# Optimization experiments

Measured on AMD Instinct MI355X. Metric: run time of the kernel, lower is better.

## Reference

```python
import math
import jax, jax.numpy as jnp
import numpy as np

B, NH, L0 = 16, 128, 16384
KS, STRIDE = 4, 2
INIT_GATE_BIAS = 1.0


def _num_steps(L, ks, stride):
    # number of reduce steps until any N <= L reaches N <= 1 (matches torch N recurrence)
    d, n = 0, L
    while True:
        n = (max(n - ks, 0) + stride - 1) // stride + 1
        d += 1
        if n <= 1:
            return d


def setup_inputs() -> dict:
    key = jax.random.key(0)
    k1, k2, k3, k4 = jax.random.split(key, 4)
    h = jax.random.normal(k1, (B, NH, L0), dtype=jnp.float32)
    N = jax.random.randint(k2, (B,), 1, L0 + 1, dtype=jnp.int32)
    cin = NH + 1  # depth_variant adds one channel
    bound = 1.0 / math.sqrt(cin * KS)
    W = jax.random.uniform(k3, (3 * NH, cin, KS), minval=-bound, maxval=bound, dtype=jnp.float32)
    b = jax.random.uniform(k4, (3 * NH,), minval=-bound, maxval=bound, dtype=jnp.float32)
    b = b.at[2 * NH:].set(INIT_GATE_BIAS)
    return {"h": h, "N": N, "W": W, "b": b}


def _step(h, N, depth, W, b):
    Bb, _, Lc = h.shape
    # depth channel (depth_variant=True), then mask invalid positions (mask applied after concat, as in torch)
    d = jnp.full((Bb, 1, Lc), math.log1p(depth), dtype=h.dtype)
    hh = jnp.concatenate([h, d], axis=1)
    mask = (jnp.arange(Lc) < N[:, None]).astype(hh.dtype)  # [B, Lc]
    hh = hh * mask[:, None, :]
    # right-pad so conv covers all valid positions
    if Lc < KS:
        pad_r = KS - Lc
    elif (Lc - KS) % STRIDE != 0:
        pad_r = STRIDE - (Lc - KS) % STRIDE
    else:
        pad_r = 0
    if pad_r:
        hh = jnp.pad(hh, ((0, 0), (0, 0), (0, pad_r)))
    lrg = jax.lax.conv_general_dilated(
        hh, W, window_strides=(STRIDE,), padding='VALID',
        dimension_numbers=('NCH', 'OIH', 'NCH')) + b[None, :, None]
    l = lrg[:, :NH]
    r = jnp.tanh(lrg[:, NH:2 * NH])
    g = jax.nn.sigmoid(lrg[:, 2 * NH:])
    h_new = l * g + r * (1.0 - g)
    m = jnp.maximum(N - KS, 0)
    N_new = (m + STRIDE - 1) // STRIDE + 1  # ceil(clamp(N-ks,0)/stride)+1
    return h_new, N_new


def reference(h, N, W, b):
    # Fixed-depth unroll: instead of compacting the batch (dynamic shapes), run
    # every sample for all D steps and record its row at the step it finishes.
    # Torch output order = samples sorted stably by finish depth (boolean-index
    # compaction preserves original relative order), reproduced via stable argsort.
    D = _num_steps(h.shape[2], KS, STRIDE)
    Bb = h.shape[0]
    out_h = jnp.zeros((Bb, NH), dtype=h.dtype)
    finish = jnp.full((Bb,), D, dtype=jnp.int32)
    done = jnp.zeros((Bb,), dtype=bool)
    for depth in range(D):
        h, N = _step(h, N, depth, W, b)
        newly = (~done) & (N <= 1)
        out_h = jnp.where(newly[:, None], h[:, :, 0], out_h)
        finish = jnp.where(newly, depth, finish)
        done = done | newly
    order = jnp.argsort(finish)  # stable by default in jax
    return out_h[order]
```

## Files before the change

kernel.cpp:

```cpp
#include <hip/hip_runtime.h>
#include <math.h>

typedef _Float16 f16_t;
typedef _Float16 f16x8 __attribute__((ext_vector_type(8)));
typedef _Float16 f16x4 __attribute__((ext_vector_type(4)));
typedef float    f32x4 __attribute__((ext_vector_type(4)));

#define NHC 128
#define NBATCH 16
#define JT 64
#define THREADS 512
#define L0LEN 16384
#define LDSROWPITCH 272
#define LDSREGION (66*LDSROWPITCH)
#define TREGION (130*LDSROWPITCH)

__device__ __host__ __forceinline__ int nstep_f(int n){ int m = n - 4; m = m < 0 ? 0 : m; return ((m + 1) >> 1) + 1; }

__global__ void prep_kernel(const float* __restrict__ W, const float* __restrict__ bin,
                            f16_t* __restrict__ Wt, float* __restrict__ Pp, float* __restrict__ biasf)
{
    int c = blockIdx.x;
    int i = threadIdx.x;
    #pragma unroll
    for (int k = 0; k < 4; k++)
        Wt[((size_t)k*384 + c)*128 + i] = (f16_t)W[((size_t)c*129 + i)*4 + k];
    if (i == 0) {
        float s = 0.f;
        Pp[c*5 + 0] = 0.f;
        #pragma unroll
        for (int k = 0; k < 4; k++) { s += W[((size_t)c*129 + 128)*4 + k]; Pp[c*5 + k + 1] = s; }
        biasf[c] = bin[c];
    }
}

template<int REG, int CTM>
__device__ __forceinline__ void gemm_tap(f32x4 (&acc)[3][4], const f16_t* __restrict__ Wt,
                                         const char* ldsIn, int arow, int n16, int q, int jt)
{
    #pragma unroll 1
    for (int k = 0; k < 4; k++) {
        const f16_t* ab = Wt + ((size_t)k*384 + arow)*128 + q*8;
        f16x8 a0[4], a1[4], a2[4];
        #pragma unroll
        for (int kc = 0; kc < 4; kc++) {
            a0[kc] = *(const f16x8*)(ab + kc*32);
            a1[kc] = *(const f16x8*)(ab + 16384 + kc*32);
            a2[kc] = *(const f16x8*)(ab + 32768 + kc*32);
        }
        const char* bb0 = ldsIn + (k&1)*REG + ((k>>1) + n16 + jt*16)*LDSROWPITCH + q*16;
        #pragma unroll
        for (int kc = 0; kc < 4; kc++) {
            #pragma unroll
            for (int ct = 0; ct < CTM; ct++) {
                f16x8 bb = *(const f16x8*)(bb0 + ct*(16*LDSROWPITCH) + kc*64);
                acc[0][ct] = __builtin_amdgcn_mfma_f32_16x16x32_f16(a0[kc], bb, acc[0][ct], 0, 0, 0);
                acc[1][ct] = __builtin_amdgcn_mfma_f32_16x16x32_f16(a1[kc], bb, acc[1][ct], 0, 0, 0);
                acc[2][ct] = __builtin_amdgcn_mfma_f32_16x16x32_f16(a2[kc], bb, acc[2][ct], 0, 0, 0);
            }
        }
    }
}

__device__ __forceinline__ void load_biasp(float (&biasr)[3][4], float (&pfull)[3][4],
                                           const float* __restrict__ biasf,
                                           const float* __restrict__ Pp, int cw)
{
    #pragma unroll
    for (int s = 0; s < 3; s++)
        #pragma unroll
        for (int r = 0; r < 4; r++) {
            int row = s*128 + cw + r;
            biasr[s][r] = biasf[row];
            pfull[s][r] = Pp[row*5 + 4];
        }
}

template<int REG, int CTE, bool TO_LDS>
__device__ __forceinline__ void epilogue_store(
    const f32x4 (&acc)[3][4], char* ldsOut, f16_t* goutB,
    const float (&biasr)[3][4], const float (&pfull)[3][4],
    const float* __restrict__ Pp, float* __restrict__ outrow,
    int j0, int Nt, int Nt1, float dval, bool record, int n16, int cw)
{
    #pragma unroll
    for (int ct = 0; ct < CTE; ct++) {
        int j = j0 + ct*16 + n16;
        int cnt = Nt - 2*j; cnt = cnt < 0 ? 0 : (cnt > 4 ? 4 : cnt);
        bool zero = (j >= Nt1);
        float hv[4];
        #pragma unroll
        for (int r = 0; r < 4; r++) {
            float d0, d1, d2;
            if (cnt == 4)      { d0 = pfull[0][r]; d1 = pfull[1][r]; d2 = pfull[2][r]; }
            else if (cnt == 0) { d0 = 0.f; d1 = 0.f; d2 = 0.f; }
            else { int rw = cw + r; d0 = Pp[rw*5 + cnt]; d1 = Pp[(128+rw)*5 + cnt]; d2 = Pp[(256+rw)*5 + cnt]; }
            float lv = acc[0][ct][r] + biasr[0][r] + dval*d0;
            float rp = acc[1][ct][r] + biasr[1][r] + dval*d1;
            float gp = acc[2][ct][r] + biasr[2][r] + dval*d2;
            float e2 = __expf(2.f*rp);
            float rv = 1.f - 2.f/(e2 + 1.f);
            float gv = 1.f/(1.f + __expf(-gp));
            float hh = lv*gv + rv*(1.f - gv);
            hv[r] = zero ? 0.f : hh;
        }
        f16x4 hb;
        #pragma unroll
        for (int r = 0; r < 4; r++) hb[r] = (f16_t)hv[r];
        if constexpr (TO_LDS) {
            *(f16x4*)(ldsOut + (j&1)*REG + (j>>1)*LDSROWPITCH + cw*2) = hb;
        } else {
            *(f16x4*)(goutB + (ct*16 + n16)*NHC + cw) = hb;
        }
        if (record && ct == 0 && n16 == 0) {
            #pragma unroll
            for (int r = 0; r < 4; r++) outrow[cw + r] = hv[r];
        }
    }
}

__global__ __launch_bounds__(THREADS) void conv_kernel(
    const float* __restrict__ h, const f16_t* __restrict__ Xin, f16_t* __restrict__ Xout,
    const f16_t* __restrict__ Wt, const float* __restrict__ Pp,
    const float* __restrict__ biasf, const int* __restrict__ N0,
    float* __restrict__ outbuf,
    int t, int inCols, int outCols, float dval)
{
    __shared__ alignas(16) char ldsX[2*LDSREGION];
    const int b  = blockIdx.y;
    const int j0 = blockIdx.x * JT;
    const int tid = threadIdx.x;
    int Nt = N0[b];
    for (int s = 0; s < t; s++) Nt = nstep_f(Nt);
    const int Nt1 = nstep_f(Nt);

    f16_t* XoutB = Xout + ((size_t)b*outCols + j0)*NHC;
    if (j0 >= Nt1) {
        float4 z = {0.f,0.f,0.f,0.f};
        float4* p = (float4*)XoutB;
        #pragma unroll
        for (int i = 0; i < 2; i++) p[i*THREADS + tid] = z;
        return;
    }

    if (t == 0) {
        const float* hB = h + (size_t)b*NHC*L0LEN;
        const int P0 = 2*j0;
        const int jpr = tid & 63;
        const int s8  = tid >> 6;
        #pragma unroll
        for (int cg = 0; cg < 16; cg++) {
            int c = cg*8 + s8;
            int p = P0 + jpr*2;
            float2 v = {0.f, 0.f};
            if (p + 1 < Nt)      v = *(const float2*)(hB + (size_t)c*L0LEN + p);
            else if (p < Nt)     v.x = hB[(size_t)c*L0LEN + p];
            char* wb = ldsX + jpr*LDSROWPITCH + c*2;
            *(f16_t*)(wb)             = (f16_t)v.x;
            *(f16_t*)(wb + LDSREGION) = (f16_t)v.y;
        }
        if (tid < 128) {
            int c = tid;
            int p = P0 + 128;
            float2 v = {0.f, 0.f};
            if (p + 1 < Nt)      v = *(const float2*)(hB + (size_t)c*L0LEN + p);
            else if (p < Nt)     v.x = hB[(size_t)c*L0LEN + p];
            char* wb = ldsX + 64*LDSROWPITCH + c*2;
            *(f16_t*)(wb)             = (f16_t)v.x;
            *(f16_t*)(wb + LDSREGION) = (f16_t)v.y;
        }
    } else {
        const char* XinB = (const char*)(Xin + ((size_t)b*inCols + 2*(size_t)j0)*NHC);
        const int maxrow = inCols - 2*j0;
        for (int it = 0; it < 5; ++it) {
            int idx = it*THREADS + tid;
            if (idx < 130*16) {
                int row = idx >> 4, cb = (idx & 15) * 16;
                float4 v = {0.f,0.f,0.f,0.f};
                if (row < maxrow) v = *(const float4*)(XinB + row*256 + cb);
                *(float4*)(ldsX + (row&1)*LDSREGION + (row>>1)*LDSROWPITCH + cb) = v;
            }
        }
    }
    __syncthreads();

    const int w    = tid >> 6;
    const int lane = tid & 63;
    const int n16  = lane & 15;
    const int q    = lane >> 4;
    const int arow = w*16 + n16;
    const int cw   = w*16 + q*4;

    f32x4 acc[3][4] = {};
    int ctm = (Nt1 - j0 + 15) >> 4; if (ctm > 4) ctm = 4;
    switch (ctm) {
    case 1:  gemm_tap<LDSREGION,1>(acc, Wt, ldsX, arow, n16, q, 0); break;
    case 2:  gemm_tap<LDSREGION,2>(acc, Wt, ldsX, arow, n16, q, 0); break;
    case 3:  gemm_tap<LDSREGION,3>(acc, Wt, ldsX, arow, n16, q, 0); break;
    default: gemm_tap<LDSREGION,4>(acc, Wt, ldsX, arow, n16, q, 0); break;
    }

    float biasr[3][4], pfull[3][4];
    load_biasp(biasr, pfull, biasf, Pp, cw);

    bool newly = (Nt1 == 1) && (t == 0 || Nt > 1);
    epilogue_store<LDSREGION,4,false>(acc, nullptr, XoutB, biasr, pfull, Pp, outbuf + b*NHC,
                                      j0, Nt, Nt1, dval, newly && (j0 == 0), n16, cw);
}

template<int REG, int CTM>
__device__ __forceinline__ void tail_iter(
    char* ldsX, const f16_t* __restrict__ Wt,
    const float (&biasr)[3][4], const float (&pfull)[3][4],
    const float* __restrict__ Pp, float* __restrict__ outrow,
    int n16, int q, int arow, int cw, int jt, int Nt, int Nt1, float dval, bool newly)
{
    f32x4 acc[3][4] = {};
    gemm_tap<REG,CTM>(acc, Wt, ldsX, arow, n16, q, jt);
    __syncthreads();
    epilogue_store<REG,CTM,true>(acc, ldsX, nullptr, biasr, pfull, Pp, outrow,
                                 jt*16, Nt, Nt1, dval, newly, n16, cw);
}

__global__ __launch_bounds__(THREADS) void tail_kernel(
    const f16_t* __restrict__ Xin, const f16_t* __restrict__ Wt,
    const float* __restrict__ Pp, const float* __restrict__ biasf,
    const int* __restrict__ N0, float* __restrict__ outbuf, int inCols)
{
    __shared__ alignas(16) char ldsX[2*TREGION];
    const int b = blockIdx.x;
    const int tid = threadIdx.x;
    int Nt = N0[b];
    for (int s = 0; s < 6; s++) Nt = nstep_f(Nt);
    if (Nt <= 1) return;

    const int w    = tid >> 6;
    const int lane = tid & 63;
    const int n16  = lane & 15;
    const int q    = lane >> 4;
    const int arow = w*16 + n16;
    const int cw   = w*16 + q*4;
    float* outrow  = outbuf + b*NHC;

    const char* XinB = (const char*)(Xin + (size_t)b*inCols*NHC);
    for (int it = 0; it < 8; ++it) {
        int idx = it*THREADS + tid;
        int row = idx >> 4, cb = (idx & 15) * 16;
        float4 v = {0.f,0.f,0.f,0.f};
        if (row < inCols) v = *(const float4*)(XinB + row*256 + cb);
        *(float4*)(ldsX + (row&1)*TREGION + (row>>1)*LDSROWPITCH + cb) = v;
    }

    float biasr[3][4], pfull[3][4];
    load_biasp(biasr, pfull, biasf, Pp, cw);
    __syncthreads();

    for (int t = 6; t < 13; ++t) {
        int Nt1 = nstep_f(Nt);
        bool newly = (Nt1 == 1);
        float dval = log1pf((float)t);
        int ctmax = (Nt1 >> 4) + 1; if (ctmax > 8) ctmax = 8;
        int cA = ctmax > 4 ? 4 : ctmax;
        switch (cA) {
        case 1:  tail_iter<TREGION,1>(ldsX, Wt, biasr, pfull, Pp, outrow, n16, q, arow, cw, 0, Nt, Nt1, dval, newly); break;
        case 2:  tail_iter<TREGION,2>(ldsX, Wt, biasr, pfull, Pp, outrow, n16, q, arow, cw, 0, Nt, Nt1, dval, newly); break;
        case 3:  tail_iter<TREGION,3>(ldsX, Wt, biasr, pfull, Pp, outrow, n16, q, arow, cw, 0, Nt, Nt1, dval, newly); break;
        default: tail_iter<TREGION,4>(ldsX, Wt, biasr, pfull, Pp, outrow, n16, q, arow, cw, 0, Nt, Nt1, dval, newly); break;
        }
        if (ctmax > 4) {
            switch (ctmax - 4) {
            case 1:  tail_iter<TREGION,1>(ldsX, Wt, biasr, pfull, Pp, outrow, n16, q, arow, cw, 4, Nt, Nt1, dval, false); break;
            case 2:  tail_iter<TREGION,2>(ldsX, Wt, biasr, pfull, Pp, outrow, n16, q, arow, cw, 4, Nt, Nt1, dval, false); break;
            case 3:  tail_iter<TREGION,3>(ldsX, Wt, biasr, pfull, Pp, outrow, n16, q, arow, cw, 4, Nt, Nt1, dval, false); break;
            default: tail_iter<TREGION,4>(ldsX, Wt, biasr, pfull, Pp, outrow, n16, q, arow, cw, 4, Nt, Nt1, dval, false); break;
            }
        }
        if (newly) return;
        Nt = Nt1;
        __syncthreads();
    }
}

__global__ void finalize_kernel(const float* __restrict__ outbuf,
                                const int* __restrict__ N0, float* __restrict__ dout)
{
    __shared__ int fin[16];
    __shared__ int rnk[16];
    int tid = threadIdx.x;
    if (tid < 16) {
        int n = N0[tid]; int f = 12;
        for (int t = 0; t < 13; t++) { n = nstep_f(n); if (n == 1) { f = t; break; } }
        fin[tid] = f;
    }
    __syncthreads();
    if (tid < 16) {
        int r = 0;
        for (int b2 = 0; b2 < 16; b2++)
            if (fin[b2] < fin[tid] || (fin[b2] == fin[tid] && b2 < tid)) r++;
        rnk[tid] = r;
    }
    __syncthreads();
    for (int e = tid; e < NBATCH*NHC; e += 256) {
        int b = e >> 7, c = e & 127;
        dout[rnk[b]*NHC + c] = outbuf[e];
    }
}

extern "C" void kernel_launch(void* const* d_in, const int* in_sizes, int n_in,
                              void* d_out, int out_size, void* d_ws, size_t ws_size,
                              hipStream_t stream)
{
    const float* h    = (const float*)d_in[0];
    const int*   N0   = (const int*)d_in[1];
    const float* W    = (const float*)d_in[2];
    const float* bvec = (const float*)d_in[3];
    float* dout = (float*)d_out;

    int Ls[14], Ms[14];
    Ls[0] = L0LEN;
    for (int t = 0; t < 13; t++) Ls[t+1] = nstep_f(Ls[t]);
    for (int t = 0; t < 14; t++) Ms[t] = ((Ls[t] + 63) / 64) * 64;

    char* ws = (char*)d_ws;
    size_t off = 0;
    auto alloc = [&](size_t bytes){ size_t o = off; off += (bytes + 255) & ~(size_t)255; return o; };
    size_t oXA   = alloc((size_t)NBATCH * Ms[1] * NHC * 2);
    size_t oXB   = alloc((size_t)NBATCH * Ms[2] * NHC * 2);
    size_t oWt   = alloc((size_t)4*384*128*2);
    size_t oPp   = alloc((size_t)384*5*4);
    size_t oBias = alloc((size_t)384*4);
    size_t oOut  = alloc((size_t)NBATCH*NHC*4);
    f16_t* XA    = (f16_t*)(ws + oXA);
    f16_t* XB    = (f16_t*)(ws + oXB);
    f16_t* Wt    = (f16_t*)(ws + oWt);
    float* Pp    = (float*)(ws + oPp);
    float* biasf = (float*)(ws + oBias);
    float* outb  = (float*)(ws + oOut);

    hipLaunchKernelGGL(prep_kernel, dim3(384), dim3(128), 0, stream, W, bvec, Wt, Pp, biasf);

    f16_t* cur = XA; f16_t* nxt = XB;
    hipLaunchKernelGGL(conv_kernel, dim3(Ms[1]/64, NBATCH), dim3(THREADS), 0, stream,
                       h, (const f16_t*)nullptr, XA, Wt, Pp, biasf, N0, outb,
                       0, Ms[0], Ms[1], log1pf(0.f));
    for (int t = 1; t < 6; t++) {
        hipLaunchKernelGGL(conv_kernel, dim3(Ms[t+1]/64, NBATCH), dim3(THREADS), 0, stream,
                           h, cur, nxt, Wt, Pp, biasf, N0, outb, t, Ms[t], Ms[t+1], log1pf((float)t));
        f16_t* tmp = cur; cur = nxt; nxt = tmp;
    }
    hipLaunchKernelGGL(tail_kernel, dim3(NBATCH), dim3(THREADS), 0, stream,
                       cur, Wt, Pp, biasf, N0, outb, Ms[6]);
    hipLaunchKernelGGL(finalize_kernel, dim3(1), dim3(256), 0, stream, outb, N0, dout);
}
```

Measured before the change: 487.1 us.

## Double column tile to 128, software-pipeline weight loads, vectorize t0 input staging

The column tile per block grows from 64 to 128 outputs with 8 accumulator tiles, so each weight fragment loaded from global is reused across twice as many MFMA columns. The tap loop becomes a two-buffer pipeline that loads the next tap's weights while issuing MFMAs for the current one. The first-step input load now packs 8 channels per thread into f16x8 LDS stores, and launch bounds request 2 blocks per SM. The cost is more registers (acc[3][8] plus two weight buffers), which may cause spills or lower occupancy, and fewer, larger blocks for the short late steps.

Result: slower. 511.1 us (+4.9%).

```diff
diff --git a/kernel.cpp b/kernel.cpp
--- a/kernel.cpp
+++ b/kernel.cpp
@@ -8,11 +8,10 @@
 
 #define NHC 128
 #define NBATCH 16
-#define JT 64
+#define JT 128
 #define THREADS 512
 #define L0LEN 16384
 #define LDSROWPITCH 272
-#define LDSREGION (66*LDSROWPITCH)
 #define TREGION (130*LDSROWPITCH)
 
 __device__ __host__ __forceinline__ int nstep_f(int n){ int m = n - 4; m = m < 0 ? 0 : m; return ((m + 1) >> 1) + 1; }
@@ -34,32 +33,37 @@
     }
 }
 
-template<int REG, int CTM>
-__device__ __forceinline__ void gemm_tap(f32x4 (&acc)[3][4], const f16_t* __restrict__ Wt,
-                                         const char* ldsIn, int arow, int n16, int q, int jt)
-{
-    #pragma unroll 1
-    for (int k = 0; k < 4; k++) {
+template<int CTM>
+__device__ __forceinline__ void gemm_pipe(f32x4 (&acc)[3][8], const f16_t* __restrict__ Wt,
+                                          const char* ldsIn, int arow, int n16, int q, int jt)
+{
+    f16x8 Xa[3][4], Xb[3][4];
+    auto loadtap = [&](f16x8 (&X)[3][4], int k){
         const f16_t* ab = Wt + ((size_t)k*384 + arow)*128 + q*8;
-        f16x8 a0[4], a1[4], a2[4];
         #pragma unroll
         for (int kc = 0; kc < 4; kc++) {
-            a0[kc] = *(const f16x8*)(ab + kc*32);
-            a1[kc] = *(const f16x8*)(ab + 16384 + kc*32);
-            a2[kc] = *(const f16x8*)(ab + 32768 + kc*32);
-        }
-        const char* bb0 = ldsIn + (k&1)*REG + ((k>>1) + n16 + jt*16)*LDSROWPITCH + q*16;
-        #pragma unroll
-        for (int kc = 0; kc < 4; kc++) {
+            X[0][kc] = *(const f16x8*)(ab + kc*32);
+            X[1][kc] = *(const f16x8*)(ab + 16384 + kc*32);
+            X[2][kc] = *(const f16x8*)(ab + 32768 + kc*32);
+        }
+    };
+    auto mfmatap = [&](const f16x8 (&X)[3][4], int k){
+        const char* bb0 = ldsIn + (k&1)*TREGION + ((k>>1) + n16 + jt*16)*LDSROWPITCH + q*16;
+        #pragma unroll
+        for (int kc = 0; kc < 4; kc++)
             #pragma unroll
             for (int ct = 0; ct < CTM; ct++) {
                 f16x8 bb = *(const f16x8*)(bb0 + ct*(16*LDSROWPITCH) + kc*64);
-                acc[0][ct] = __builtin_amdgcn_mfma_f32_16x16x32_f16(a0[kc], bb, acc[0][ct], 0, 0, 0);
-                acc[1][ct] = __builtin_amdgcn_mfma_f32_16x16x32_f16(a1[kc], bb, acc[1][ct], 0, 0, 0);
-                acc[2][ct] = __builtin_amdgcn_mfma_f32_16x16x32_f16(a2[kc], bb, acc[2][ct], 0, 0, 0);
+                acc[0][ct] = __builtin_amdgcn_mfma_f32_16x16x32_f16(X[0][kc], bb, acc[0][ct], 0, 0, 0);
+                acc[1][ct] = __builtin_amdgcn_mfma_f32_16x16x32_f16(X[1][kc], bb, acc[1][ct], 0, 0, 0);
+                acc[2][ct] = __builtin_amdgcn_mfma_f32_16x16x32_f16(X[2][kc], bb, acc[2][ct], 0, 0, 0);
             }
-        }
-    }
+    };
+    loadtap(Xa, 0);
+    loadtap(Xb, 1);  mfmatap(Xa, 0);
+    loadtap(Xa, 2);  mfmatap(Xb, 1);
+    loadtap(Xb, 3);  mfmatap(Xa, 2);
+                     mfmatap(Xb, 3);
 }
 
 __device__ __forceinline__ void load_biasp(float (&biasr)[3][4], float (&pfull)[3][4],
@@ -76,9 +80,9 @@
         }
 }
 
-template<int REG, int CTE, bool TO_LDS>
+template<int CTE, bool TO_LDS>
 __device__ __forceinline__ void epilogue_store(
-    const f32x4 (&acc)[3][4], char* ldsOut, f16_t* goutB,
+    const f32x4 (&acc)[3][8], char* ldsOut, f16_t* goutB,
     const float (&biasr)[3][4], const float (&pfull)[3][4],
     const float* __restrict__ Pp, float* __restrict__ outrow,
     int j0, int Nt, int Nt1, float dval, bool record, int n16, int cw)
@@ -108,7 +112,7 @@
         #pragma unroll
         for (int r = 0; r < 4; r++) hb[r] = (f16_t)hv[r];
         if constexpr (TO_LDS) {
-            *(f16x4*)(ldsOut + (j&1)*REG + (j>>1)*LDSROWPITCH + cw*2) = hb;
+            *(f16x4*)(ldsOut + (j&1)*TREGION + (j>>1)*LDSROWPITCH + cw*2) = hb;
         } else {
             *(f16x4*)(goutB + (ct*16 + n16)*NHC + cw) = hb;
         }
@@ -119,14 +123,14 @@
     }
 }
 
-__global__ __launch_bounds__(THREADS) void conv_kernel(
+__global__ __launch_bounds__(THREADS, 2) void conv_kernel(
     const float* __restrict__ h, const f16_t* __restrict__ Xin, f16_t* __restrict__ Xout,
     const f16_t* __restrict__ Wt, const float* __restrict__ Pp,
     const float* __restrict__ biasf, const int* __restrict__ N0,
     float* __restrict__ outbuf,
     int t, int inCols, int outCols, float dval)
 {
-    __shared__ alignas(16) char ldsX[2*LDSREGION];
+    __shared__ alignas(16) char ldsX[2*TREGION];
     const int b  = blockIdx.y;
     const int j0 = blockIdx.x * JT;
     const int tid = threadIdx.x;
@@ -139,46 +143,51 @@
         float4 z = {0.f,0.f,0.f,0.f};
         float4* p = (float4*)XoutB;
         #pragma unroll
-        for (int i = 0; i < 2; i++) p[i*THREADS + tid] = z;
+        for (int i = 0; i < 4; i++) p[i*THREADS + tid] = z;
         return;
     }
 
     if (t == 0) {
         const float* hB = h + (size_t)b*NHC*L0LEN;
         const int P0 = 2*j0;
-        const int jpr = tid & 63;
-        const int s8  = tid >> 6;
-        #pragma unroll
-        for (int cg = 0; cg < 16; cg++) {
-            int c = cg*8 + s8;
-            int p = P0 + jpr*2;
+        const int s4 = tid >> 7;
+        const int pr = tid & 127;
+        const int p  = P0 + pr*2;
+        const bool full = (p + 1 < Nt), half = (p < Nt);
+        #pragma unroll 1
+        for (int g = 0; g < 4; g++) {
+            int cbase = s4*32 + g*8;
+            f16x8 ev, od;
+            #pragma unroll
+            for (int e = 0; e < 8; e++) {
+                float2 v = {0.f, 0.f};
+                if (full)      v = *(const float2*)(hB + (size_t)(cbase + e)*L0LEN + p);
+                else if (half) v.x = hB[(size_t)(cbase + e)*L0LEN + p];
+                ev[e] = (f16_t)v.x; od[e] = (f16_t)v.y;
+            }
+            char* wb = ldsX + pr*LDSROWPITCH + cbase*2;
+            *(f16x8*)(wb)           = ev;
+            *(f16x8*)(wb + TREGION) = od;
+        }
+        if (tid < 128) {
+            int c = tid, pe = P0 + 256;
             float2 v = {0.f, 0.f};
-            if (p + 1 < Nt)      v = *(const float2*)(hB + (size_t)c*L0LEN + p);
-            else if (p < Nt)     v.x = hB[(size_t)c*L0LEN + p];
-            char* wb = ldsX + jpr*LDSROWPITCH + c*2;
-            *(f16_t*)(wb)             = (f16_t)v.x;
-            *(f16_t*)(wb + LDSREGION) = (f16_t)v.y;
-        }
-        if (tid < 128) {
-            int c = tid;
-            int p = P0 + 128;
-            float2 v = {0.f, 0.f};
-            if (p + 1 < Nt)      v = *(const float2*)(hB + (size_t)c*L0LEN + p);
-            else if (p < Nt)     v.x = hB[(size_t)c*L0LEN + p];
-            char* wb = ldsX + 64*LDSROWPITCH + c*2;
-            *(f16_t*)(wb)             = (f16_t)v.x;
-            *(f16_t*)(wb + LDSREGION) = (f16_t)v.y;
+            if (pe + 1 < Nt)  v = *(const float2*)(hB + (size_t)c*L0LEN + pe);
+            else if (pe < Nt) v.x = hB[(size_t)c*L0LEN + pe];
+            char* wb = ldsX + 128*LDSROWPITCH + c*2;
+            *(f16_t*)(wb)           = (f16_t)v.x;
+            *(f16_t*)(wb + TREGION) = (f16_t)v.y;
         }
     } else {
         const char* XinB = (const char*)(Xin + ((size_t)b*inCols + 2*(size_t)j0)*NHC);
         const int maxrow = inCols - 2*j0;
-        for (int it = 0; it < 5; ++it) {
+        for (int it = 0; it < 9; ++it) {
             int idx = it*THREADS + tid;
-            if (idx < 130*16) {
+            if (idx < 258*16) {
                 int row = idx >> 4, cb = (idx & 15) * 16;
                 float4 v = {0.f,0.f,0.f,0.f};
                 if (row < maxrow) v = *(const float4*)(XinB + row*256 + cb);
-                *(float4*)(ldsX + (row&1)*LDSREGION + (row>>1)*LDSROWPITCH + cb) = v;
+                *(float4*)(ldsX + (row&1)*TREGION + (row>>1)*LDSROWPITCH + cb) = v;
             }
         }
     }
@@ -191,38 +200,42 @@
     const int arow = w*16 + n16;
     const int cw   = w*16 + q*4;
 
-    f32x4 acc[3][4] = {};
-    int ctm = (Nt1 - j0 + 15) >> 4; if (ctm > 4) ctm = 4;
+    f32x4 acc[3][8] = {};
+    int ctm = (Nt1 - j0 + 15) >> 4; if (ctm > 8) ctm = 8;
     switch (ctm) {
-    case 1:  gemm_tap<LDSREGION,1>(acc, Wt, ldsX, arow, n16, q, 0); break;
-    case 2:  gemm_tap<LDSREGION,2>(acc, Wt, ldsX, arow, n16, q, 0); break;
-    case 3:  gemm_tap<LDSREGION,3>(acc, Wt, ldsX, arow, n16, q, 0); break;
-    default: gemm_tap<LDSREGION,4>(acc, Wt, ldsX, arow, n16, q, 0); break;
+    case 1:  gemm_pipe<1>(acc, Wt, ldsX, arow, n16, q, 0); break;
+    case 2:  gemm_pipe<2>(acc, Wt, ldsX, arow, n16, q, 0); break;
+    case 3:  gemm_pipe<3>(acc, Wt, ldsX, arow, n16, q, 0); break;
+    case 4:  gemm_pipe<4>(acc, Wt, ldsX, arow, n16, q, 0); break;
+    case 5:  gemm_pipe<5>(acc, Wt, ldsX, arow, n16, q, 0); break;
+    case 6:  gemm_pipe<6>(acc, Wt, ldsX, arow, n16, q, 0); break;
+    case 7:  gemm_pipe<7>(acc, Wt, ldsX, arow, n16, q, 0); break;
+    default: gemm_pipe<8>(acc, Wt, ldsX, arow, n16, q, 0); break;
     }
 
     float biasr[3][4], pfull[3][4];
     load_biasp(biasr, pfull, biasf, Pp, cw);
 
     bool newly = (Nt1 == 1) && (t == 0 || Nt > 1);
-    epilogue_store<LDSREGION,4,false>(acc, nullptr, XoutB, biasr, pfull, Pp, outbuf + b*NHC,
-                                      j0, Nt, Nt1, dval, newly && (j0 == 0), n16, cw);
-}
-
-template<int REG, int CTM>
+    epilogue_store<8, false>(acc, nullptr, XoutB, biasr, pfull, Pp, outbuf + b*NHC,
+                             j0, Nt, Nt1, dval, newly && (j0 == 0), n16, cw);
+}
+
+template<int CTM>
 __device__ __forceinline__ void tail_iter(
     char* ldsX, const f16_t* __restrict__ Wt,
     const float (&biasr)[3][4], const float (&pfull)[3][4],
     const float* __restrict__ Pp, float* __restrict__ outrow,
     int n16, int q, int arow, int cw, int jt, int Nt, int Nt1, float dval, bool newly)
 {
-    f32x4 acc[3][4] = {};
-    gemm_tap<REG,CTM>(acc, Wt, ldsX, arow, n16, q, jt);
-    __syncthreads();
-    epilogue_store<REG,CTM,true>(acc, ldsX, nullptr, biasr, pfull, Pp, outrow,
-                                 jt*16, Nt, Nt1, dval, newly, n16, cw);
-}
-
-__global__ __launch_bounds__(THREADS) void tail_kernel(
+    f32x4 acc[3][8] = {};
+    gemm_pipe<CTM>(acc, Wt, ldsX, arow, n16, q, jt);
+    __syncthreads();
+    epilogue_store<CTM, true>(acc, ldsX, nullptr, biasr, pfull, Pp, outrow,
+                              jt*16, Nt, Nt1, dval, newly, n16, cw);
+}
+
+__global__ __launch_bounds__(THREADS, 2) void tail_kernel(
     const f16_t* __restrict__ Xin, const f16_t* __restrict__ Wt,
     const float* __restrict__ Pp, const float* __restrict__ biasf,
     const int* __restrict__ N0, float* __restrict__ outbuf, int inCols)
@@ -262,17 +275,17 @@
         int ctmax = (Nt1 >> 4) + 1; if (ctmax > 8) ctmax = 8;
         int cA = ctmax > 4 ? 4 : ctmax;
         switch (cA) {
-        case 1:  tail_iter<TREGION,1>(ldsX, Wt, biasr, pfull, Pp, outrow, n16, q, arow, cw, 0, Nt, Nt1, dval, newly); break;
-        case 2:  tail_iter<TREGION,2>(ldsX, Wt, biasr, pfull, Pp, outrow, n16, q, arow, cw, 0, Nt, Nt1, dval, newly); break;
-        case 3:  tail_iter<TREGION,3>(ldsX, Wt, biasr, pfull, Pp, outrow, n16, q, arow, cw, 0, Nt, Nt1, dval, newly); break;
-        default: tail_iter<TREGION,4>(ldsX, Wt, biasr, pfull, Pp, outrow, n16, q, arow, cw, 0, Nt, Nt1, dval, newly); break;
+        case 1:  tail_iter<1>(ldsX, Wt, biasr, pfull, Pp, outrow, n16, q, arow, cw, 0, Nt, Nt1, dval, newly); break;
+        case 2:  tail_iter<2>(ldsX, Wt, biasr, pfull, Pp, outrow, n16, q, arow, cw, 0, Nt, Nt1, dval, newly); break;
+        case 3:  tail_iter<3>(ldsX, Wt, biasr, pfull, Pp, outrow, n16, q, arow, cw, 0, Nt, Nt1, dval, newly); break;
+        default: tail_iter<4>(ldsX, Wt, biasr, pfull, Pp, outrow, n16, q, arow, cw, 0, Nt, Nt1, dval, newly); break;
         }
         if (ctmax > 4) {
             switch (ctmax - 4) {
-            case 1:  tail_iter<TREGION,1>(ldsX, Wt, biasr, pfull, Pp, outrow, n16, q, arow, cw, 4, Nt, Nt1, dval, false); break;
-            case 2:  tail_iter<TREGION,2>(ldsX, Wt, biasr, pfull, Pp, outrow, n16, q, arow, cw, 4, Nt, Nt1, dval, false); break;
-            case 3:  tail_iter<TREGION,3>(ldsX, Wt, biasr, pfull, Pp, outrow, n16, q, arow, cw, 4, Nt, Nt1, dval, false); break;
-            default: tail_iter<TREGION,4>(ldsX, Wt, biasr, pfull, Pp, outrow, n16, q, arow, cw, 4, Nt, Nt1, dval, false); break;
+            case 1:  tail_iter<1>(ldsX, Wt, biasr, pfull, Pp, outrow, n16, q, arow, cw, 4, Nt, Nt1, dval, false); break;
+            case 2:  tail_iter<2>(ldsX, Wt, biasr, pfull, Pp, outrow, n16, q, arow, cw, 4, Nt, Nt1, dval, false); break;
+            case 3:  tail_iter<3>(ldsX, Wt, biasr, pfull, Pp, outrow, n16, q, arow, cw, 4, Nt, Nt1, dval, false); break;
+            default: tail_iter<4>(ldsX, Wt, biasr, pfull, Pp, outrow, n16, q, arow, cw, 4, Nt, Nt1, dval, false); break;
             }
         }
         if (newly) return;
@@ -319,7 +332,7 @@
     int Ls[14], Ms[14];
     Ls[0] = L0LEN;
     for (int t = 0; t < 13; t++) Ls[t+1] = nstep_f(Ls[t]);
-    for (int t = 0; t < 14; t++) Ms[t] = ((Ls[t] + 63) / 64) * 64;
+    for (int t = 0; t < 14; t++) Ms[t] = ((Ls[t] + 127) / 128) * 128;
 
     char* ws = (char*)d_ws;
     size_t off = 0;
@@ -340,11 +353,11 @@
     hipLaunchKernelGGL(prep_kernel, dim3(384), dim3(128), 0, stream, W, bvec, Wt, Pp, biasf);
 
     f16_t* cur = XA; f16_t* nxt = XB;
-    hipLaunchKernelGGL(conv_kernel, dim3(Ms[1]/64, NBATCH), dim3(THREADS), 0, stream,
+    hipLaunchKernelGGL(conv_kernel, dim3(Ms[1]/JT, NBATCH), dim3(THREADS), 0, stream,
                        h, (const f16_t*)nullptr, XA, Wt, Pp, biasf, N0, outb,
                        0, Ms[0], Ms[1], log1pf(0.f));
     for (int t = 1; t < 6; t++) {
-        hipLaunchKernelGGL(conv_kernel, dim3(Ms[t+1]/64, NBATCH), dim3(THREADS), 0, stream,
+        hipLaunchKernelGGL(conv_kernel, dim3(Ms[t+1]/JT, NBATCH), dim3(THREADS), 0, stream,
                            h, cur, nxt, Wt, Pp, biasf, N0, outb, t, Ms[t], Ms[t+1], log1pf((float)t));
         f16_t* tmp = cur; cur = nxt; nxt = tmp;
     }
```

## Keep tail weights in registers, shrink tail block, trim dead-tile zeroing

Applied to the files above, without the earlier changes.

The tail kernel now runs with 256 threads. Each wave preloads its full set of weight fragments for two row groups into registers once, instead of reloading them from global memory on every tap and iteration. Bias and depth-correction tables are staged in LDS, and the tail processes 16-column panels in a simple loop rather than template-dispatched chunks. In conv_kernel, out-of-range blocks now zero only the small boundary region next to the valid range instead of their whole tile. This cuts global traffic at the cost of heavy register pressure and less parallelism in the tail.

Result: faster. 438.6 us (median of 2 runs) (-10.0%).

```diff
diff --git a/kernel.cpp b/kernel.cpp
--- a/kernel.cpp
+++ b/kernel.cpp
@@ -10,10 +10,11 @@
 #define NBATCH 16
 #define JT 64
 #define THREADS 512
+#define TTHREADS 256
 #define L0LEN 16384
 #define LDSROWPITCH 272
 #define LDSREGION (66*LDSROWPITCH)
-#define TREGION (130*LDSROWPITCH)
+#define TREG (130*LDSROWPITCH)
 
 __device__ __host__ __forceinline__ int nstep_f(int n){ int m = n - 4; m = m < 0 ? 0 : m; return ((m + 1) >> 1) + 1; }
 
@@ -34,9 +35,9 @@
     }
 }
 
-template<int REG, int CTM>
+template<int CTM>
 __device__ __forceinline__ void gemm_tap(f32x4 (&acc)[3][4], const f16_t* __restrict__ Wt,
-                                         const char* ldsIn, int arow, int n16, int q, int jt)
+                                         const char* ldsIn, int arow, int n16, int q)
 {
     #pragma unroll 1
     for (int k = 0; k < 4; k++) {
@@ -48,7 +49,7 @@
             a1[kc] = *(const f16x8*)(ab + 16384 + kc*32);
             a2[kc] = *(const f16x8*)(ab + 32768 + kc*32);
         }
-        const char* bb0 = ldsIn + (k&1)*REG + ((k>>1) + n16 + jt*16)*LDSROWPITCH + q*16;
+        const char* bb0 = ldsIn + (k&1)*LDSREGION + ((k>>1) + n16)*LDSROWPITCH + q*16;
         #pragma unroll
         for (int kc = 0; kc < 4; kc++) {
             #pragma unroll
@@ -76,15 +77,96 @@
         }
 }
 
-template<int REG, int CTE, bool TO_LDS>
-__device__ __forceinline__ void epilogue_store(
-    const f32x4 (&acc)[3][4], char* ldsOut, f16_t* goutB,
-    const float (&biasr)[3][4], const float (&pfull)[3][4],
-    const float* __restrict__ Pp, float* __restrict__ outrow,
-    int j0, int Nt, int Nt1, float dval, bool record, int n16, int cw)
-{
-    #pragma unroll
-    for (int ct = 0; ct < CTE; ct++) {
+__global__ __launch_bounds__(THREADS) void conv_kernel(
+    const float* __restrict__ h, const f16_t* __restrict__ Xin, f16_t* __restrict__ Xout,
+    const f16_t* __restrict__ Wt, const float* __restrict__ Pp,
+    const float* __restrict__ biasf, const int* __restrict__ N0,
+    float* __restrict__ outbuf,
+    int t, int inCols, int outCols, float dval)
+{
+    __shared__ alignas(16) char ldsX[2*LDSREGION];
+    const int b  = blockIdx.y;
+    const int j0 = blockIdx.x * JT;
+    const int tid = threadIdx.x;
+    int Nt = N0[b];
+    for (int s = 0; s < t; s++) Nt = nstep_f(Nt);
+    const int Nt1 = nstep_f(Nt);
+
+    f16_t* XoutB = Xout + ((size_t)b*outCols + j0)*NHC;
+    if (j0 >= Nt1) {
+        if (j0 <= Nt1 + 1 && tid < 32) {
+            float4 z = {0.f,0.f,0.f,0.f};
+            ((float4*)XoutB)[tid] = z;
+        }
+        return;
+    }
+
+    if (t == 0) {
+        const float* hB = h + (size_t)b*NHC*L0LEN;
+        const int P0 = 2*j0;
+        const int jpr = tid & 63;
+        const int s8  = tid >> 6;
+        #pragma unroll
+        for (int cg = 0; cg < 16; cg++) {
+            int c = cg*8 + s8;
+            int p = P0 + jpr*2;
+            float2 v = {0.f, 0.f};
+            if (p + 1 < Nt)      v = *(const float2*)(hB + (size_t)c*L0LEN + p);
+            else if (p < Nt)     v.x = hB[(size_t)c*L0LEN + p];
+            char* wb = ldsX + jpr*LDSROWPITCH + c*2;
+            *(f16_t*)(wb)             = (f16_t)v.x;
+            *(f16_t*)(wb + LDSREGION) = (f16_t)v.y;
+        }
+        if (tid < 128) {
+            int c = tid;
+            int p = P0 + 128;
+            float2 v = {0.f, 0.f};
+            if (p + 1 < Nt)      v = *(const float2*)(hB + (size_t)c*L0LEN + p);
+            else if (p < Nt)     v.x = hB[(size_t)c*L0LEN + p];
+            char* wb = ldsX + 64*LDSROWPITCH + c*2;
+            *(f16_t*)(wb)             = (f16_t)v.x;
+            *(f16_t*)(wb + LDSREGION) = (f16_t)v.y;
+        }
+    } else {
+        const char* XinB = (const char*)(Xin + ((size_t)b*inCols + 2*(size_t)j0)*NHC);
+        const int maxrow = inCols - 2*j0;
+        for (int it = 0; it < 5; ++it) {
+            int idx = it*THREADS + tid;
+            if (idx < 130*16) {
+                int row = idx >> 4, cb = (idx & 15) * 16;
+                float4 v = {0.f,0.f,0.f,0.f};
+                if (row < maxrow) v = *(const float4*)(XinB + row*256 + cb);
+                *(float4*)(ldsX + (row&1)*LDSREGION + (row>>1)*LDSROWPITCH + cb) = v;
+            }
+        }
+    }
+    __syncthreads();
+
+    const int w    = tid >> 6;
+    const int lane = tid & 63;
+    const int n16  = lane & 15;
+    const int q    = lane >> 4;
+    const int arow = w*16 + n16;
+    const int cw   = w*16 + q*4;
+
+    f32x4 acc[3][4] = {};
+    int ctm = (Nt1 - j0 + 15) >> 4; if (ctm > 4) ctm = 4;
+    switch (ctm) {
+    case 1:  gemm_tap<1>(acc, Wt, ldsX, arow, n16, q); break;
+    case 2:  gemm_tap<2>(acc, Wt, ldsX, arow, n16, q); break;
+    case 3:  gemm_tap<3>(acc, Wt, ldsX, arow, n16, q); break;
+    default: gemm_tap<4>(acc, Wt, ldsX, arow, n16, q); break;
+    }
+
+    float biasr[3][4], pfull[3][4];
+    load_biasp(biasr, pfull, biasf, Pp, cw);
+
+    bool newly = (Nt1 == 1) && (t == 0 || Nt > 1);
+    bool record = newly && (j0 == 0);
+    float* outrow = outbuf + b*NHC;
+
+    #pragma unroll
+    for (int ct = 0; ct < 4; ct++) {
         int j = j0 + ct*16 + n16;
         int cnt = Nt - 2*j; cnt = cnt < 0 ? 0 : (cnt > 4 ? 4 : cnt);
         bool zero = (j >= Nt1);
@@ -107,11 +189,7 @@
         f16x4 hb;
         #pragma unroll
         for (int r = 0; r < 4; r++) hb[r] = (f16_t)hv[r];
-        if constexpr (TO_LDS) {
-            *(f16x4*)(ldsOut + (j&1)*REG + (j>>1)*LDSROWPITCH + cw*2) = hb;
-        } else {
-            *(f16x4*)(goutB + (ct*16 + n16)*NHC + cw) = hb;
-        }
+        *(f16x4*)(XoutB + (ct*16 + n16)*NHC + cw) = hb;
         if (record && ct == 0 && n16 == 0) {
             #pragma unroll
             for (int r = 0; r < 4; r++) outrow[cw + r] = hv[r];
@@ -119,118 +197,18 @@
     }
 }
 
-__global__ __launch_bounds__(THREADS) void conv_kernel(
-    const float* __restrict__ h, const f16_t* __restrict__ Xin, f16_t* __restrict__ Xout,
-    const f16_t* __restrict__ Wt, const float* __restrict__ Pp,
-    const float* __restrict__ biasf, const int* __restrict__ N0,
-    float* __restrict__ outbuf,
-    int t, int inCols, int outCols, float dval)
-{
-    __shared__ alignas(16) char ldsX[2*LDSREGION];
-    const int b  = blockIdx.y;
-    const int j0 = blockIdx.x * JT;
-    const int tid = threadIdx.x;
-    int Nt = N0[b];
-    for (int s = 0; s < t; s++) Nt = nstep_f(Nt);
-    const int Nt1 = nstep_f(Nt);
-
-    f16_t* XoutB = Xout + ((size_t)b*outCols + j0)*NHC;
-    if (j0 >= Nt1) {
-        float4 z = {0.f,0.f,0.f,0.f};
-        float4* p = (float4*)XoutB;
-        #pragma unroll
-        for (int i = 0; i < 2; i++) p[i*THREADS + tid] = z;
-        return;
-    }
-
-    if (t == 0) {
-        const float* hB = h + (size_t)b*NHC*L0LEN;
-        const int P0 = 2*j0;
-        const int jpr = tid & 63;
-        const int s8  = tid >> 6;
-        #pragma unroll
-        for (int cg = 0; cg < 16; cg++) {
-            int c = cg*8 + s8;
-            int p = P0 + jpr*2;
-            float2 v = {0.f, 0.f};
-            if (p + 1 < Nt)      v = *(const float2*)(hB + (size_t)c*L0LEN + p);
-            else if (p < Nt)     v.x = hB[(size_t)c*L0LEN + p];
-            char* wb = ldsX + jpr*LDSROWPITCH + c*2;
-            *(f16_t*)(wb)             = (f16_t)v.x;
-            *(f16_t*)(wb + LDSREGION) = (f16_t)v.y;
-        }
-        if (tid < 128) {
-            int c = tid;
-            int p = P0 + 128;
-            float2 v = {0.f, 0.f};
-            if (p + 1 < Nt)      v = *(const float2*)(hB + (size_t)c*L0LEN + p);
-            else if (p < Nt)     v.x = hB[(size_t)c*L0LEN + p];
-            char* wb = ldsX + 64*LDSROWPITCH + c*2;
-            *(f16_t*)(wb)             = (f16_t)v.x;
-            *(f16_t*)(wb + LDSREGION) = (f16_t)v.y;
-        }
-    } else {
-        const char* XinB = (const char*)(Xin + ((size_t)b*inCols + 2*(size_t)j0)*NHC);
-        const int maxrow = inCols - 2*j0;
-        for (int it = 0; it < 5; ++it) {
-            int idx = it*THREADS + tid;
-            if (idx < 130*16) {
-                int row = idx >> 4, cb = (idx & 15) * 16;
-                float4 v = {0.f,0.f,0.f,0.f};
-                if (row < maxrow) v = *(const float4*)(XinB + row*256 + cb);
-                *(float4*)(ldsX + (row&1)*LDSREGION + (row>>1)*LDSROWPITCH + cb) = v;
-            }
-        }
-    }
-    __syncthreads();
-
-    const int w    = tid >> 6;
-    const int lane = tid & 63;
-    const int n16  = lane & 15;
-    const int q    = lane >> 4;
-    const int arow = w*16 + n16;
-    const int cw   = w*16 + q*4;
-
-    f32x4 acc[3][4] = {};
-    int ctm = (Nt1 - j0 + 15) >> 4; if (ctm > 4) ctm = 4;
-    switch (ctm) {
-    case 1:  gemm_tap<LDSREGION,1>(acc, Wt, ldsX, arow, n16, q, 0); break;
-    case 2:  gemm_tap<LDSREGION,2>(acc, Wt, ldsX, arow, n16, q, 0); break;
-    case 3:  gemm_tap<LDSREGION,3>(acc, Wt, ldsX, arow, n16, q, 0); break;
-    default: gemm_tap<LDSREGION,4>(acc, Wt, ldsX, arow, n16, q, 0); break;
-    }
-
-    float biasr[3][4], pfull[3][4];
-    load_biasp(biasr, pfull, biasf, Pp, cw);
-
-    bool newly = (Nt1 == 1) && (t == 0 || Nt > 1);
-    epilogue_store<LDSREGION,4,false>(acc, nullptr, XoutB, biasr, pfull, Pp, outbuf + b*NHC,
-                                      j0, Nt, Nt1, dval, newly && (j0 == 0), n16, cw);
-}
-
-template<int REG, int CTM>
-__device__ __forceinline__ void tail_iter(
-    char* ldsX, const f16_t* __restrict__ Wt,
-    const float (&biasr)[3][4], const float (&pfull)[3][4],
-    const float* __restrict__ Pp, float* __restrict__ outrow,
-    int n16, int q, int arow, int cw, int jt, int Nt, int Nt1, float dval, bool newly)
-{
-    f32x4 acc[3][4] = {};
-    gemm_tap<REG,CTM>(acc, Wt, ldsX, arow, n16, q, jt);
-    __syncthreads();
-    epilogue_store<REG,CTM,true>(acc, ldsX, nullptr, biasr, pfull, Pp, outrow,
-                                 jt*16, Nt, Nt1, dval, newly, n16, cw);
-}
-
-__global__ __launch_bounds__(THREADS) void tail_kernel(
+__global__ __launch_bounds__(TTHREADS, 1) void tail_kernel(
     const f16_t* __restrict__ Xin, const f16_t* __restrict__ Wt,
     const float* __restrict__ Pp, const float* __restrict__ biasf,
     const int* __restrict__ N0, float* __restrict__ outbuf, int inCols)
 {
-    __shared__ alignas(16) char ldsX[2*TREGION];
+    __shared__ alignas(16) char ldsX[2*TREG + (384 + 1920)*4];
+    float* ldsBias = (float*)(ldsX + 2*TREG);
+    float* ldsPp   = ldsBias + 384;
     const int b = blockIdx.x;
     const int tid = threadIdx.x;
     int Nt = N0[b];
+    #pragma unroll
     for (int s = 0; s < 6; s++) Nt = nstep_f(Nt);
     if (Nt <= 1) return;
 
@@ -242,37 +220,85 @@
     const int cw   = w*16 + q*4;
     float* outrow  = outbuf + b*NHC;
 
+    f16x8 A[2][4][4][3];
+    #pragma unroll
+    for (int rg = 0; rg < 2; rg++) {
+        #pragma unroll
+        for (int k = 0; k < 4; k++) {
+            const f16_t* ab = Wt + ((size_t)k*384 + arow + rg*64)*128 + q*8;
+            #pragma unroll
+            for (int kc = 0; kc < 4; kc++) {
+                A[rg][k][kc][0] = *(const f16x8*)(ab + kc*32);
+                A[rg][k][kc][1] = *(const f16x8*)(ab + 16384 + kc*32);
+                A[rg][k][kc][2] = *(const f16x8*)(ab + 32768 + kc*32);
+            }
+        }
+    }
+
     const char* XinB = (const char*)(Xin + (size_t)b*inCols*NHC);
-    for (int it = 0; it < 8; ++it) {
-        int idx = it*THREADS + tid;
-        int row = idx >> 4, cb = (idx & 15) * 16;
-        float4 v = {0.f,0.f,0.f,0.f};
-        if (row < inCols) v = *(const float4*)(XinB + row*256 + cb);
-        *(float4*)(ldsX + (row&1)*TREGION + (row>>1)*LDSROWPITCH + cb) = v;
-    }
-
-    float biasr[3][4], pfull[3][4];
-    load_biasp(biasr, pfull, biasf, Pp, cw);
+    for (int it = 0; it < 17; ++it) {
+        int idx = it*TTHREADS + tid;
+        if (idx < 258*16) {
+            int row = idx >> 4, cb = (idx & 15) * 16;
+            float4 v = {0.f,0.f,0.f,0.f};
+            if (row < inCols) v = *(const float4*)(XinB + row*256 + cb);
+            *(float4*)(ldsX + (row&1)*TREG + (row>>1)*LDSROWPITCH + cb) = v;
+        }
+    }
+    for (int i = tid; i < 384;  i += TTHREADS) ldsBias[i] = biasf[i];
+    for (int i = tid; i < 1920; i += TTHREADS) ldsPp[i]   = Pp[i];
     __syncthreads();
 
     for (int t = 6; t < 13; ++t) {
         int Nt1 = nstep_f(Nt);
         bool newly = (Nt1 == 1);
         float dval = log1pf((float)t);
-        int ctmax = (Nt1 >> 4) + 1; if (ctmax > 8) ctmax = 8;
-        int cA = ctmax > 4 ? 4 : ctmax;
-        switch (cA) {
-        case 1:  tail_iter<TREGION,1>(ldsX, Wt, biasr, pfull, Pp, outrow, n16, q, arow, cw, 0, Nt, Nt1, dval, newly); break;
-        case 2:  tail_iter<TREGION,2>(ldsX, Wt, biasr, pfull, Pp, outrow, n16, q, arow, cw, 0, Nt, Nt1, dval, newly); break;
-        case 3:  tail_iter<TREGION,3>(ldsX, Wt, biasr, pfull, Pp, outrow, n16, q, arow, cw, 0, Nt, Nt1, dval, newly); break;
-        default: tail_iter<TREGION,4>(ldsX, Wt, biasr, pfull, Pp, outrow, n16, q, arow, cw, 0, Nt, Nt1, dval, newly); break;
-        }
-        if (ctmax > 4) {
-            switch (ctmax - 4) {
-            case 1:  tail_iter<TREGION,1>(ldsX, Wt, biasr, pfull, Pp, outrow, n16, q, arow, cw, 4, Nt, Nt1, dval, false); break;
-            case 2:  tail_iter<TREGION,2>(ldsX, Wt, biasr, pfull, Pp, outrow, n16, q, arow, cw, 4, Nt, Nt1, dval, false); break;
-            case 3:  tail_iter<TREGION,3>(ldsX, Wt, biasr, pfull, Pp, outrow, n16, q, arow, cw, 4, Nt, Nt1, dval, false); break;
-            default: tail_iter<TREGION,4>(ldsX, Wt, biasr, pfull, Pp, outrow, n16, q, arow, cw, 4, Nt, Nt1, dval, false); break;
+        int np = (Nt1 >> 4) + 1; if (np > 8) np = 8;
+        for (int p = 0; p < np; ++p) {
+            f32x4 acc[2][3] = {};
+            #pragma unroll
+            for (int k = 0; k < 4; k++) {
+                const char* bb0 = ldsX + (k&1)*TREG + ((k>>1) + p*16 + n16)*LDSROWPITCH + q*16;
+                #pragma unroll
+                for (int kc = 0; kc < 4; kc++) {
+                    f16x8 bb = *(const f16x8*)(bb0 + kc*64);
+                    #pragma unroll
+                    for (int rg = 0; rg < 2; rg++) {
+                        acc[rg][0] = __builtin_amdgcn_mfma_f32_16x16x32_f16(A[rg][k][kc][0], bb, acc[rg][0], 0, 0, 0);
+                        acc[rg][1] = __builtin_amdgcn_mfma_f32_16x16x32_f16(A[rg][k][kc][1], bb, acc[rg][1], 0, 0, 0);
+                        acc[rg][2] = __builtin_amdgcn_mfma_f32_16x16x32_f16(A[rg][k][kc][2], bb, acc[rg][2], 0, 0, 0);
+                    }
+                }
+            }
+            __syncthreads();
+
+            int j = p*16 + n16;
+            int cnt = Nt - 2*j; cnt = cnt < 0 ? 0 : (cnt > 4 ? 4 : cnt);
+            bool zero = (j >= Nt1);
+            #pragma unroll
+            for (int rg = 0; rg < 2; rg++) {
+                int cwr = cw + rg*64;
+                float hv[4];
+                #pragma unroll
+                for (int r = 0; r < 4; r++) {
+                    int row = cwr + r;
+                    float lv = acc[rg][0][r] + ldsBias[row]       + dval*ldsPp[row*5 + cnt];
+                    float rp = acc[rg][1][r] + ldsBias[128 + row] + dval*ldsPp[(128 + row)*5 + cnt];
+                    float gp = acc[rg][2][r] + ldsBias[256 + row] + dval*ldsPp[(256 + row)*5 + cnt];
+                    float e2 = __expf(2.f*rp);
+                    float rv = 1.f - 2.f/(e2 + 1.f);
+                    float gv = 1.f/(1.f + __expf(-gp));
+                    float hh = lv*gv + rv*(1.f - gv);
+                    hv[r] = zero ? 0.f : hh;
+                }
+                f16x4 hb;
+                #pragma unroll
+                for (int r = 0; r < 4; r++) hb[r] = (f16_t)hv[r];
+                *(f16x4*)(ldsX + (j&1)*TREG + (j>>1)*LDSROWPITCH + cwr*2) = hb;
+                if (newly && p == 0 && n16 == 0) {
+                    #pragma unroll
+                    for (int r = 0; r < 4; r++) outrow[cwr + r] = hv[r];
+                }
             }
         }
         if (newly) return;
@@ -340,15 +366,15 @@
     hipLaunchKernelGGL(prep_kernel, dim3(384), dim3(128), 0, stream, W, bvec, Wt, Pp, biasf);
 
     f16_t* cur = XA; f16_t* nxt = XB;
-    hipLaunchKernelGGL(conv_kernel, dim3(Ms[1]/64, NBATCH), dim3(THREADS), 0, stream,
+    hipLaunchKernelGGL(conv_kernel, dim3(Ms[1]/JT, NBATCH), dim3(THREADS), 0, stream,
                        h, (const f16_t*)nullptr, XA, Wt, Pp, biasf, N0, outb,
                        0, Ms[0], Ms[1], log1pf(0.f));
     for (int t = 1; t < 6; t++) {
-        hipLaunchKernelGGL(conv_kernel, dim3(Ms[t+1]/64, NBATCH), dim3(THREADS), 0, stream,
+        hipLaunchKernelGGL(conv_kernel, dim3(Ms[t+1]/JT, NBATCH), dim3(THREADS), 0, stream,
                            h, cur, nxt, Wt, Pp, biasf, N0, outb, t, Ms[t], Ms[t+1], log1pf((float)t));
         f16_t* tmp = cur; cur = nxt; nxt = tmp;
     }
-    hipLaunchKernelGGL(tail_kernel, dim3(NBATCH), dim3(THREADS), 0, stream,
+    hipLaunchKernelGGL(tail_kernel, dim3(NBATCH), dim3(TTHREADS), 0, stream,
                        cur, Wt, Pp, biasf, N0, outb, Ms[6]);
     hipLaunchKernelGGL(finalize_kernel, dim3(1), dim3(256), 0, stream, outb, N0, dout);
 }
```
